# Optimization experiments

Hardware: AMD Instinct MI355X
Metric: run time of the kernel (lower is better)

Reference implementation:

```python
import jax, jax.numpy as jnp
import numpy as np

D_MODEL = 512; NHEAD = 8; D_FF = 2048
B = 8; C = 64; P = 128
HALF = D_MODEL // 2        # per-branch embed dim (256)
H_HALF = NHEAD // 2        # per-branch heads (4)
HD = HALF // H_HALF        # per-branch head dim (64)
ROPE_BASE = 10000.0
THETA_SCALE = 2.0 * np.pi
LN_EPS = 1e-5; RMS_EPS = 1e-8


def setup_inputs():
    ks = jax.random.split(jax.random.key(0), 16)
    w = lambda k, s: jax.random.normal(k, s, jnp.float32) * 0.02
    return {
        "src": jax.random.normal(ks[0], (B, C, P, D_MODEL), jnp.float32),
        "coords": jax.random.normal(ks[1], (C, 3), jnp.float32),
        "q_attn": w(ks[2], (D_MODEL,)), "rms_attn": jnp.ones((D_MODEL,), jnp.float32),
        "proj_attn_w": w(ks[3], (D_MODEL, D_MODEL)), "proj_attn_b": jnp.zeros((D_MODEL,), jnp.float32),
        "q_ffn": w(ks[4], (D_MODEL,)), "rms_ffn": jnp.ones((D_MODEL,), jnp.float32),
        "proj_ffn_w": w(ks[5], (D_MODEL, D_MODEL)), "proj_ffn_b": jnp.zeros((D_MODEL,), jnp.float32),
        "ln1_w": jnp.ones((D_MODEL,), jnp.float32), "ln1_b": jnp.zeros((D_MODEL,), jnp.float32),
        "ln2_w": jnp.ones((D_MODEL,), jnp.float32), "ln2_b": jnp.zeros((D_MODEL,), jnp.float32),
        "qkv_s_w": w(ks[6], (3 * HALF, HALF)), "qkv_s_b": jnp.zeros((3 * HALF,), jnp.float32),
        "out_s_w": w(ks[7], (HALF, HALF)), "out_s_b": jnp.zeros((HALF,), jnp.float32),
        "qkv_t_w": w(ks[8], (3 * HALF, HALF)), "qkv_t_b": jnp.zeros((3 * HALF,), jnp.float32),
        "out_t_w": w(ks[9], (HALF, HALF)), "out_t_b": jnp.zeros((HALF,), jnp.float32),
        "w1": w(ks[10], (D_FF, D_MODEL)), "b1": jnp.zeros((D_FF,), jnp.float32),
        "w2": w(ks[11], (D_MODEL, D_FF)), "b2": jnp.zeros((D_MODEL,), jnp.float32),
    }


def _rmsnorm(x, w):
    return x / jnp.sqrt(jnp.mean(x * x, axis=-1, keepdims=True) + RMS_EPS) * w


def _layernorm(x, w, b):
    m = jnp.mean(x, axis=-1, keepdims=True)
    v = jnp.mean((x - m) ** 2, axis=-1, keepdims=True)
    return (x - m) / jnp.sqrt(v + LN_EPS) * w + b


def _attn_residual(src, q, norm_w, proj_w, proj_b):
    # sources = [src] stacked on a leading n-axis (n=1) as in AttentionResidual
    V = src[None]                                  # (n, B, C, P, D)
    K = _rmsnorm(V, norm_w)
    logits = jnp.einsum('d,nbcpd->nbcp', q, K)
    wgt = jax.nn.softmax(logits, axis=0)
    out = jnp.einsum('nbcp,nbcpd->bcpd', wgt, V)
    return out @ proj_w.T + proj_b


def _build_freqs(half, dtype):
    idx = jnp.arange(half, dtype=dtype)
    return 1.0 / ROPE_BASE ** (idx / max(half, 1))


def _coord_rope(coords, half):
    # coords: (L, 3); returns cos, sin of shape (1, 1, L, half)
    axis_ids = jnp.arange(half) % 3
    c = coords - jnp.mean(coords, axis=0, keepdims=True)
    r = jnp.linalg.norm(c, axis=-1)
    c = c / jnp.maximum(jnp.max(r), 1e-6)
    freqs = _build_freqs(half, coords.dtype)
    theta = THETA_SCALE * (c[:, axis_ids] * freqs[None, :])   # (L, half)
    return jnp.cos(theta)[None, None], jnp.sin(theta)[None, None]


def _index_rope(L, half, dtype):
    freqs = _build_freqs(half, dtype)
    pos = jnp.arange(L, dtype=dtype)[:, None]
    theta = pos * freqs[None, :]                               # (L, half)
    return jnp.cos(theta)[None, None], jnp.sin(theta)[None, None]


def _apply_rope(q, k, cos, sin):
    half = q.shape[-1] // 2
    q1, q2 = q[..., :half], q[..., half:]
    k1, k2 = k[..., :half], k[..., half:]
    qr = jnp.concatenate([q1 * cos - q2 * sin, q1 * sin + q2 * cos], axis=-1)
    kr = jnp.concatenate([k1 * cos - k2 * sin, k1 * sin + k2 * cos], axis=-1)
    return qr, kr


def _mha(x, w_qkv, b_qkv, w_o, b_o, H, cos, sin):
    Bx, L, E = x.shape
    Hd = E // H
    qkv = x @ w_qkv.T + b_qkv
    q, k, v = jnp.split(qkv, 3, axis=-1)
    q = q.reshape(Bx, L, H, Hd).transpose(0, 2, 1, 3)   # (B, H, L, Hd)
    k = k.reshape(Bx, L, H, Hd).transpose(0, 2, 1, 3)
    v = v.reshape(Bx, L, H, Hd).transpose(0, 2, 1, 3)
    q, k = _apply_rope(q, k, cos, sin)
    scores = jnp.einsum('bhld,bhmd->bhlm', q, k) * (Hd ** -0.5)
    attn = jax.nn.softmax(scores, axis=-1)
    out = jnp.einsum('bhlm,bhmd->bhld', attn, v)
    out = out.transpose(0, 2, 1, 3).reshape(Bx, L, E)
    return out @ w_o.T + b_o


def reference(src, coords, q_attn, rms_attn, proj_attn_w, proj_attn_b,
              q_ffn, rms_ffn, proj_ffn_w, proj_ffn_b,
              ln1_w, ln1_b, ln2_w, ln2_b,
              qkv_s_w, qkv_s_b, out_s_w, out_s_b,
              qkv_t_w, qkv_t_b, out_t_w, out_t_b,
              w1, b1, w2, b2):
    Bx, Cx, Px, D = src.shape
    half = D // 2
    # --- attention block (pre-norm, attention-residual shortcut) ---
    res1 = _attn_residual(src, q_attn, rms_attn, proj_attn_w, proj_attn_b)
    x = _layernorm(src, ln1_w, ln1_b)
    # spatial branch: attention over channels with coordinate RoPE
    xs = x[..., :half].transpose(0, 2, 1, 3).reshape(Bx * Px, Cx, half)
    cos_s, sin_s = _coord_rope(coords, HD // 2)
    ys = _mha(xs, qkv_s_w, qkv_s_b, out_s_w, out_s_b, H_HALF, cos_s, sin_s)
    ys = ys.reshape(Bx, Px, Cx, half).transpose(0, 2, 1, 3)
    # temporal branch: attention over patches with index RoPE
    xt = x[..., half:].reshape(Bx * Cx, Px, half)
    cos_t, sin_t = _index_rope(Px, HD // 2, src.dtype)
    yt = _mha(xt, qkv_t_w, qkv_t_b, out_t_w, out_t_b, H_HALF, cos_t, sin_t)
    yt = yt.reshape(Bx, Cx, Px, half)
    x = res1 + jnp.concatenate([ys, yt], axis=-1)
    # --- FFN block ---
    res2 = _attn_residual(x, q_ffn, rms_ffn, proj_ffn_w, proj_ffn_b)
    y = _layernorm(x, ln2_w, ln2_b)
    ff = jax.nn.gelu(y @ w1.T + b1, approximate=False) @ w2.T + b2
    return res2 + ff
```

## Files before the change

### kernel.cpp

```cpp
#include <hip/hip_runtime.h>
#include <math.h>
#include <type_traits>

using u16 = unsigned short;
using u32 = unsigned int;

typedef __bf16 bf16x8 __attribute__((ext_vector_type(8)));
typedef float f32x4 __attribute__((ext_vector_type(4)));

__device__ __forceinline__ float lof(u32 u) { u32 x = u << 16; float f; __builtin_memcpy(&f, &x, 4); return f; }
__device__ __forceinline__ float hif(u32 u) { u32 x = u & 0xffff0000u; float f; __builtin_memcpy(&f, &x, 4); return f; }
__device__ __forceinline__ u16 f2bf(float f) {
  u32 u; __builtin_memcpy(&u, &f, 4);
  u32 r = u + 0x7fffu + ((u >> 16) & 1u);
  return (u16)(r >> 16);
}
__device__ __forceinline__ u32 pack2(float a, float b) { return (u32)f2bf(a) | ((u32)f2bf(b) << 16); }
__device__ __forceinline__ float bf2f(u16 s) { u32 x = ((u32)s) << 16; float f; __builtin_memcpy(&f, &x, 4); return f; }
__device__ __forceinline__ float elem(const u32* arr, int j) { u32 u = arr[j >> 1]; return (j & 1) ? hif(u) : lof(u); }

__device__ __forceinline__ void gload_lds16(const u16* g, u16* l) {
  __builtin_amdgcn_global_load_lds((const __attribute__((address_space(1))) void*)g,
                                   (__attribute__((address_space(3))) void*)l, 16, 0, 0);
}

__device__ __forceinline__ float gelu_f(float x) {
  float x3 = x * x * x;
  float u = fmaf(x3, 0.07135481283f, 1.5957691216f * x);
  float e = __expf(u);
  float r = __builtin_amdgcn_rcpf(e + 1.0f);
  return x * e * r;
}

#define NTOK 65536

#define WB_PA   0
#define WB_PF   262144
#define WB_QS   524288
#define WB_QT   720896
#define WB_OS   917504
#define WB_OT   983040
#define WB_W1   1048576
#define WB_W2F  2097152
#define WB_TOT  3407872

#define UC_US 0
#define UC_CS 768
#define UC_UT 1536
#define UC_CT 2304
#define UC_U1 3072
#define UC_C1 5120
#define UC_BC 7168

constexpr size_t O_WB  = 0;
constexpr size_t O_TAB = 6815744;
constexpr size_t O_ST1 = 6864896;
constexpr size_t O_ST2 = 7389184;
constexpr size_t O_UC  = 7913472;
constexpr size_t O_X   = 7944192;
constexpr size_t O_HB  = O_X + (size_t)NTOK * 512 * 2;

__global__ __launch_bounds__(256) void convert_weights_kernel(
    const float* __restrict__ pa, const float* __restrict__ pf,
    const float* __restrict__ qs, const float* __restrict__ qt,
    const float* __restrict__ os_, const float* __restrict__ ot,
    const float* __restrict__ w1, const float* __restrict__ w2,
    const float* __restrict__ ln1w, const float* __restrict__ ln2w,
    u16* __restrict__ dst)
{
  int i = blockIdx.x * 256 + threadIdx.x;
  if (i >= WB_TOT) return;
  float v;
  if (i < 262144)       { v = pa[i]; }
  else if (i < 524288)  { v = pf[i - 262144]; }
  else if (i < 720896)  { int l = i - 524288;  v = qs[l] * ln1w[l & 255]; }
  else if (i < 917504)  { int l = i - 720896;  v = qt[l] * ln1w[256 + (l & 255)]; }
  else if (i < 983040)  { v = os_[i - 917504]; }
  else if (i < 1048576) { v = ot[i - 983040]; }
  else if (i < 2097152) { int l = i - 1048576; v = w1[l] * ln2w[l & 511]; }
  else {
    int l = i - 2097152; int row = l / 2560, col = l - row * 2560;
    v = (col < 2048) ? w2[row * 2048 + col] : pf[row * 512 + (col - 2048)];
  }
  dst[i] = f2bf(v);
}

__global__ __launch_bounds__(256) void ucvec_kernel(
    const float* __restrict__ qs, const float* __restrict__ qt, const float* __restrict__ w1,
    const float* __restrict__ ln1w, const float* __restrict__ ln1b,
    const float* __restrict__ ln2w, const float* __restrict__ ln2b,
    const float* __restrict__ b2, const float* __restrict__ pfb,
    float* __restrict__ uc)
{
  const int j = blockIdx.x * 4 + (threadIdx.x >> 6);
  const int l = threadIdx.x & 63;
  float u = 0.f, c = 0.f;
  if (j < 768) {
#pragma unroll
    for (int q = 0; q < 4; q++) {
      int k = l * 4 + q;
      float w = qs[j * 256 + k];
      u += ln1w[k] * w; c += ln1b[k] * w;
    }
  } else if (j < 1536) {
    int jj = j - 768;
#pragma unroll
    for (int q = 0; q < 4; q++) {
      int k = l * 4 + q;
      float w = qt[jj * 256 + k];
      u += ln1w[256 + k] * w; c += ln1b[256 + k] * w;
    }
  } else if (j < 3584) {
    int jj = j - 1536;
#pragma unroll
    for (int q = 0; q < 8; q++) {
      int k = l * 8 + q;
      float w = w1[jj * 512 + k];
      u += ln2w[k] * w; c += ln2b[k] * w;
    }
  } else if (j < 4096) {
    if (l == 0) { int jj = j - 3584; uc[UC_BC + jj] = b2[jj] + pfb[jj]; }
    return;
  } else return;
#pragma unroll
  for (int o = 32; o > 0; o >>= 1) { u += __shfl_xor(u, o); c += __shfl_xor(c, o); }
  if (l == 0) {
    if (j < 768)       { uc[UC_US + j] = u;          uc[UC_CS + j] = c; }
    else if (j < 1536) { uc[UC_UT + (j - 768)] = u;  uc[UC_CT + (j - 768)] = c; }
    else               { uc[UC_U1 + (j - 1536)] = u; uc[UC_C1 + (j - 1536)] = c; }
  }
}

__global__ __launch_bounds__(256) void rope_tables_kernel(const float* __restrict__ coords, float* __restrict__ tab)
{
  __shared__ float cs[192];
  __shared__ float mean3[3];
  __shared__ float rmax;
  int t = threadIdx.x;
  if (t < 192) cs[t] = coords[t];
  __syncthreads();
  if (t < 3) { float s = 0.f; for (int i = 0; i < 64; i++) s += cs[i * 3 + t]; mean3[t] = s * (1.0f / 64.0f); }
  __syncthreads();
  if (t < 192) cs[t] -= mean3[t % 3];
  __syncthreads();
  if (t == 0) {
    float mx = 0.f;
    for (int i = 0; i < 64; i++) {
      float x = cs[i * 3], y = cs[i * 3 + 1], z = cs[i * 3 + 2];
      mx = fmaxf(mx, sqrtf(x * x + y * y + z * z));
    }
    rmax = fmaxf(mx, 1e-6f);
  }
  __syncthreads();
  float inv = 1.0f / rmax;
  for (int e = t; e < 2048; e += 256) {
    int c = e >> 5, j = e & 31;
    float freq = 1.0f / powf(10000.0f, (float)j * (1.0f / 32.0f));
    float th = 6.283185307179586f * (cs[c * 3 + (j % 3)] * inv) * freq;
    tab[e] = cosf(th); tab[2048 + e] = sinf(th);
  }
  for (int e = t; e < 4096; e += 256) {
    int p = e >> 5, j = e & 31;
    float freq = 1.0f / powf(10000.0f, (float)j * (1.0f / 32.0f));
    float th = (float)p * freq;
    tab[4096 + e] = cosf(th); tab[8192 + e] = sinf(th);
  }
}

__global__ __launch_bounds__(256) void ln_stats_f32_kernel(
    const float* __restrict__ xin, float2* __restrict__ st, u16* __restrict__ srcb)
{
  const int tok = blockIdx.x * 4 + (threadIdx.x >> 6);
  const int lane = threadIdx.x & 63;
  const float* row = xin + (size_t)tok * 512 + lane * 8;
  float4 v0 = ((const float4*)row)[0];
  float4 v1 = ((const float4*)row)[1];
  float v[8] = {v0.x, v0.y, v0.z, v0.w, v1.x, v1.y, v1.z, v1.w};
  float s = 0.f, ss = 0.f;
#pragma unroll
  for (int j = 0; j < 8; j++) { s += v[j]; ss += v[j] * v[j]; }
#pragma unroll
  for (int o = 32; o > 0; o >>= 1) { s += __shfl_xor(s, o); ss += __shfl_xor(ss, o); }
  if (lane == 0) {
    float mean = s * (1.0f / 512.0f);
    float rstd = rsqrtf(ss * (1.0f / 512.0f) - mean * mean + 1e-5f);
    st[tok] = make_float2(mean, rstd);
  }
  if (srcb) {
    uint4 o; u32* op = (u32*)&o;
#pragma unroll
    for (int d = 0; d < 4; d++) op[d] = pack2(v[2 * d], v[2 * d + 1]);
    *(uint4*)(srcb + (size_t)tok * 512 + lane * 8) = o;
  }
}

__global__ __launch_bounds__(256) void ln_stats_bf16_kernel(const u16* __restrict__ xin, float2* __restrict__ st)
{
  const int tok = blockIdx.x * 4 + (threadIdx.x >> 6);
  const int lane = threadIdx.x & 63;
  uint4 u = ((const uint4*)(xin + (size_t)tok * 512))[lane];
  u32 uu[4] = {u.x, u.y, u.z, u.w};
  float s = 0.f, ss = 0.f;
#pragma unroll
  for (int d = 0; d < 4; d++) {
    float a = lof(uu[d]), b = hif(uu[d]);
    s += a + b; ss += a * a + b * b;
  }
#pragma unroll
  for (int o = 32; o > 0; o >>= 1) { s += __shfl_xor(s, o); ss += __shfl_xor(ss, o); }
  if (lane == 0) {
    float mean = s * (1.0f / 512.0f);
    float rstd = rsqrtf(ss * (1.0f / 512.0f) - mean * mean + 1e-5f);
    st[tok] = make_float2(mean, rstd);
  }
}

template<int AMODE, int EMODE, typename OutT>
__global__ __launch_bounds__(256) void gemm128_kernel(
    const u16* __restrict__ A16, int lda,
    const u16* __restrict__ A2, int lda2,
    const u16* __restrict__ Wt, int ldw,
    OutT* __restrict__ C, int ldc,
    const float* __restrict__ bias,
    const float2* __restrict__ stats,
    const float* __restrict__ uvec, const float* __restrict__ cvec,
    int K)
{
  const int t = threadIdx.x;
  const int lane = t & 63, wid = t >> 6;
  const int wm = wid >> 1, wn = wid & 1;
  const int l15 = lane & 15, l4 = lane >> 4;

  const int ntn = gridDim.x;
  const int nwg = ntn * gridDim.y;
  int flat = blockIdx.y * ntn + blockIdx.x;
  int q = nwg >> 3, rmd = nwg & 7, xcd = flat & 7, idx = flat >> 3;
  int wg = (xcd < rmd ? xcd * (q + 1) : rmd * (q + 1) + (xcd - rmd) * q) + idx;
  const int m0 = (wg / ntn) * 128, n0 = (wg % ntn) * 128;

  f32x4 acc[4][4] = {};
  const int r0 = t >> 2;
  const size_t arow0 = (size_t)(m0 + r0);

  __shared__ u16 Asb[2][128 * 32];
  __shared__ u16 Bsb[2][128 * 32];
  const int chs = (t & 3) ^ ((t >> 3) & 3);
  const u16* Wp = Wt + (size_t)(n0 + r0) * ldw + chs * 8;
  const size_t wstep = (size_t)64 * ldw;
  const int nt = K / 32;
  auto stage = [&](int ti, int buf) {
    const int kk = ti * 32;
    const int cbk = kk + chs * 8;
    const u16* pa; size_t rstep;
    if constexpr (AMODE == 4) {
      if (kk < 2048) { pa = A16 + arow0 * lda + cbk;          rstep = (size_t)64 * lda; }
      else           { pa = A2 + arow0 * lda2 + (cbk - 2048); rstep = (size_t)64 * lda2; }
    } else {
      pa = A16 + arow0 * lda + cbk; rstep = (size_t)64 * lda;
    }
    gload_lds16(pa, &Asb[buf][t * 8]);
    gload_lds16(pa + rstep, &Asb[buf][t * 8 + 2048]);
    gload_lds16(Wp + kk, &Bsb[buf][t * 8]);
    gload_lds16(Wp + wstep + kk, &Bsb[buf][t * 8 + 2048]);
  };
  stage(0, 0);
  int cur = 0;
  const int pco = (l4 ^ ((l15 >> 1) & 3)) * 8;
  for (int ti = 0; ti < nt; ti++) {
    if (ti + 1 < nt) {
      stage(ti + 1, cur ^ 1);
      __builtin_amdgcn_sched_barrier(0);
      asm volatile("s_waitcnt vmcnt(4)" ::: "memory");
    } else {
      __builtin_amdgcn_sched_barrier(0);
      asm volatile("s_waitcnt vmcnt(0)" ::: "memory");
    }
    __builtin_amdgcn_sched_barrier(0);
    __builtin_amdgcn_s_barrier();
    __builtin_amdgcn_sched_barrier(0);
    bf16x8 af[4], bfr[4];
#pragma unroll
    for (int i = 0; i < 4; i++)
      af[i] = *(const bf16x8*)(&Asb[cur][(wm * 64 + i * 16 + l15) * 32 + pco]);
#pragma unroll
    for (int j = 0; j < 4; j++)
      bfr[j] = *(const bf16x8*)(&Bsb[cur][(wn * 64 + j * 16 + l15) * 32 + pco]);
#pragma unroll
    for (int i = 0; i < 4; i++)
#pragma unroll
      for (int j = 0; j < 4; j++)
        acc[i][j] = __builtin_amdgcn_mfma_f32_16x16x32_bf16(af[i], bfr[j], acc[i][j], 0, 0, 0);
    __builtin_amdgcn_sched_barrier(0);
    __builtin_amdgcn_s_barrier();
    __builtin_amdgcn_sched_barrier(0);
    cur ^= 1;
  }

#pragma unroll
  for (int i = 0; i < 4; i++) {
    const int row = m0 + wm * 64 + i * 16 + l4 * 4;
#pragma unroll
    for (int j = 0; j < 4; j++) {
      const int col = n0 + wn * 64 + j * 16 + l15;
      const float bv = bias[col];
#pragma unroll
      for (int rr = 0; rr < 4; rr++) {
        float v = acc[i][j][rr];
        if constexpr (EMODE >= 3) {
          float2 s = stats[row + rr];
          v = s.y * v - s.x * s.y * uvec[col] + cvec[col] + bv;
          if constexpr (EMODE == 4) v = gelu_f(v);
        } else {
          v += bv;
        }
        const size_t idxc = (size_t)(row + rr) * ldc + col;
        if constexpr (std::is_same<OutT, u16>::value) {
          if constexpr (EMODE == 2) v += bf2f(C[idxc]);
          C[idxc] = f2bf(v);
        } else {
          if constexpr (EMODE == 2) v += C[idxc];
          C[idxc] = v;
        }
      }
    }
  }
}

template<int EMODE, typename OutT>
__global__ __launch_bounds__(256) void gemm_f32a_kernel(
    const float* __restrict__ A32, int lda,
    const u16* __restrict__ Wt, int ldw,
    OutT* __restrict__ C, int ldc,
    const float* __restrict__ bias,
    const float2* __restrict__ stats,
    const float* __restrict__ uvec, const float* __restrict__ cvec,
    int K)
{
  const int t = threadIdx.x;
  const int lane = t & 63, wid = t >> 6;
  const int wm = wid >> 1, wn = wid & 1;
  const int l15 = lane & 15, l4 = lane >> 4;
  const int r0 = t >> 2;
  const int ntn = gridDim.x;
  const int nwg = ntn * gridDim.y;
  int flat = blockIdx.y * ntn + blockIdx.x;
  int q = nwg >> 3, rmd = nwg & 7, xcd = flat & 7, idx = flat >> 3;
  int wg = (xcd < rmd ? xcd * (q + 1) : rmd * (q + 1) + (xcd - rmd) * q) + idx;
  const int m0 = (wg / ntn) * 128, n0 = (wg % ntn) * 128;
  f32x4 acc[4][4] = {};
  const size_t arow0 = (size_t)(m0 + r0);
  const int ch = t & 3;
  const u16* Wp = Wt + (size_t)(n0 + r0) * ldw + ch * 8;
  const size_t wstep = (size_t)64 * ldw;
  __shared__ u16 As[128 * 40];
  __shared__ u16 Bs[128 * 32];
  for (int k0 = 0; k0 < K; k0 += 32) {
    const int cbx = k0 + ch * 8;
    uint4 a0, a1;
    float f0[8], f1[8];
    float4 x0 = *(const float4*)(A32 + arow0 * lda + cbx);
    float4 x1 = *(const float4*)(A32 + arow0 * lda + cbx + 4);
    float4 y0 = *(const float4*)(A32 + (arow0 + 64) * lda + cbx);
    float4 y1 = *(const float4*)(A32 + (arow0 + 64) * lda + cbx + 4);
    f0[0]=x0.x; f0[1]=x0.y; f0[2]=x0.z; f0[3]=x0.w; f0[4]=x1.x; f0[5]=x1.y; f0[6]=x1.z; f0[7]=x1.w;
    f1[0]=y0.x; f1[1]=y0.y; f1[2]=y0.z; f1[3]=y0.w; f1[4]=y1.x; f1[5]=y1.y; f1[6]=y1.z; f1[7]=y1.w;
    u32* p0 = (u32*)&a0; u32* p1 = (u32*)&a1;
#pragma unroll
    for (int d = 0; d < 4; d++) { p0[d] = pack2(f0[2*d], f0[2*d+1]); p1[d] = pack2(f1[2*d], f1[2*d+1]); }
    __syncthreads();
    gload_lds16(Wp + k0, Bs + t * 8);
    gload_lds16(Wp + wstep + k0, Bs + t * 8 + 2048);
    *(uint4*)(As + r0 * 40 + ch * 8) = a0;
    *(uint4*)(As + (r0 + 64) * 40 + ch * 8) = a1;
    __syncthreads();
    bf16x8 af[4], bfr[4];
#pragma unroll
    for (int i = 0; i < 4; i++)
      af[i] = *(const bf16x8*)(As + (wm * 64 + i * 16 + l15) * 40 + l4 * 8);
#pragma unroll
    for (int j = 0; j < 4; j++)
      bfr[j] = *(const bf16x8*)(Bs + (wn * 64 + j * 16 + l15) * 32 + l4 * 8);
#pragma unroll
    for (int i = 0; i < 4; i++)
#pragma unroll
      for (int j = 0; j < 4; j++)
        acc[i][j] = __builtin_amdgcn_mfma_f32_16x16x32_bf16(af[i], bfr[j], acc[i][j], 0, 0, 0);
  }
#pragma unroll
  for (int i = 0; i < 4; i++) {
    const int row = m0 + wm * 64 + i * 16 + l4 * 4;
#pragma unroll
    for (int j = 0; j < 4; j++) {
      const int col = n0 + wn * 64 + j * 16 + l15;
      const float bv = bias[col];
#pragma unroll
      for (int rr = 0; rr < 4; rr++) {
        float v = acc[i][j][rr];
        if constexpr (EMODE == 3) {
          float2 s = stats[row + rr];
          v = s.y * v - s.x * s.y * uvec[col] + cvec[col] + bv;
        } else {
          v += bv;
        }
        const size_t idxc = (size_t)(row + rr) * ldc + col;
        if constexpr (std::is_same<OutT, u16>::value) C[idxc] = f2bf(v);
        else C[idxc] = v;
      }
    }
  }
}

template<int L>
__global__ __launch_bounds__(256) void attn_mfma_kernel(
    const u16* __restrict__ qkv,
    u16* __restrict__ aout,
    const float* __restrict__ tab)
{
  constexpr int KP = 72;
  constexpr int PP = L + 8;
  constexpr int VP = L + 8;
  constexpr int NI = L / 64;
  constexpr int NJ = L / 16;
  constexpr int NK = L / 32;
  __shared__ u16 Ks[L * KP];
  __shared__ u16 Vt[64 * VP];
  __shared__ u16 Ps[L * PP];

  const int t = threadIdx.x;
  const int lane = t & 63;
  const int w = t >> 6;
  const int l15 = lane & 15, l4 = lane >> 4;
  const int sq = blockIdx.x, h = blockIdx.y;

  long base; int tstride; const float *ct, *st;
  if constexpr (L == 64) { base = (long)(sq >> 7) * 8192 + (sq & 127); tstride = 128; ct = tab;        st = tab + 2048; }
  else                   { base = (long)sq * 128;                      tstride = 1;   ct = tab + 4096; st = tab + 8192; }

  {
    const int tok = t >> 1, hh = t & 1;
    if (tok < L) {
      const size_t rb = (size_t)(base + (long)tok * tstride) * 768 + h * 64;
      u32 ku[32];
#pragma unroll
      for (int i = 0; i < 8; i++) ((uint4*)ku)[i] = ((const uint4*)(qkv + rb + 256))[i];
      const float* cc = ct + tok * 32;
      const float* ss = st + tok * 32;
      u32* kd = (u32*)(Ks + tok * KP + hh * 32);
#pragma unroll
      for (int jj = 0; jj < 16; jj++) {
        float c0 = cc[2*jj], s0 = ss[2*jj], c1 = cc[2*jj+1], s1 = ss[2*jj+1];
        float a0 = elem(ku, 2*jj),     b0 = elem(ku, 2*jj+32);
        float a1 = elem(ku, 2*jj+1),   b1 = elem(ku, 2*jj+33);
        float r0v = hh ? (a0*s0 + b0*c0) : (a0*c0 - b0*s0);
        float r1v = hh ? (a1*s1 + b1*c1) : (a1*c1 - b1*s1);
        kd[jj] = pack2(r0v, r1v);
      }
      u32 vu[16];
#pragma unroll
      for (int i = 0; i < 4; i++) ((uint4*)vu)[i] = ((const uint4*)(qkv + rb + 512 + hh * 32))[i];
#pragma unroll
      for (int j = 0; j < 32; j++)
        Vt[(hh * 32 + j) * VP + tok] = (u16)(vu[j >> 1] >> ((j & 1) * 16));
    }
  }

  bf16x8 aq[NI][2];
#pragma unroll
  for (int i = 0; i < NI; i++) {
    const int row = w * (16 * NI) + i * 16 + l15;
    const u16* qr = qkv + (size_t)(base + (long)row * tstride) * 768 + h * 64;
    uint4 ua = *(const uint4*)(qr + l4 * 8);
    uint4 ub = *(const uint4*)(qr + 32 + l4 * 8);
    u32 au[4] = {ua.x, ua.y, ua.z, ua.w};
    u32 bu[4] = {ub.x, ub.y, ub.z, ub.w};
    const float* cc = ct + row * 32 + l4 * 8;
    const float* ss = st + row * 32 + l4 * 8;
    u32 q0[4], q1[4];
#pragma unroll
    for (int d = 0; d < 4; d++) {
      float a0 = lof(au[d]), a1 = hif(au[d]);
      float b0 = lof(bu[d]), b1 = hif(bu[d]);
      float c0 = cc[2*d], c1 = cc[2*d+1], s0 = ss[2*d], s1 = ss[2*d+1];
      q0[d] = pack2(a0*c0 - b0*s0, a1*c1 - b1*s1);
      q1[d] = pack2(a0*s0 + b0*c0, a1*s1 + b1*c1);
    }
    __builtin_memcpy(&aq[i][0], q0, 16);
    __builtin_memcpy(&aq[i][1], q1, 16);
  }
  __syncthreads();

  f32x4 acc[NI][NJ] = {};
#pragma unroll
  for (int j = 0; j < NJ; j++) {
#pragma unroll
    for (int kk = 0; kk < 2; kk++) {
      bf16x8 bk = *(const bf16x8*)(Ks + (j * 16 + l15) * KP + kk * 32 + l4 * 8);
#pragma unroll
      for (int i = 0; i < NI; i++)
        acc[i][j] = __builtin_amdgcn_mfma_f32_16x16x32_bf16(aq[i][kk], bk, acc[i][j], 0, 0, 0);
    }
  }

  float inv_[NI][4];
#pragma unroll
  for (int i = 0; i < NI; i++) {
#pragma unroll
    for (int rr = 0; rr < 4; rr++) {
      float m = acc[i][0][rr];
#pragma unroll
      for (int j = 1; j < NJ; j++) m = fmaxf(m, acc[i][j][rr]);
      m = fmaxf(m, __shfl_xor(m, 1)); m = fmaxf(m, __shfl_xor(m, 2));
      m = fmaxf(m, __shfl_xor(m, 4)); m = fmaxf(m, __shfl_xor(m, 8));
      m *= 0.125f;
      const int qrow = w * (16 * NI) + i * 16 + l4 * 4 + rr;
      float sm = 0.f;
#pragma unroll
      for (int j = 0; j < NJ; j++) {
        float e = __expf(acc[i][j][rr] * 0.125f - m);
        sm += e;
        Ps[qrow * PP + j * 16 + l15] = f2bf(e);
      }
      sm += __shfl_xor(sm, 1); sm += __shfl_xor(sm, 2);
      sm += __shfl_xor(sm, 4); sm += __shfl_xor(sm, 8);
      inv_[i][rr] = 1.0f / sm;
    }
  }

  f32x4 o[NI][4] = {};
#pragma unroll
  for (int kk = 0; kk < NK; kk++) {
    bf16x8 pa[NI];
#pragma unroll
    for (int i = 0; i < NI; i++)
      pa[i] = *(const bf16x8*)(Ps + (w * (16 * NI) + i * 16 + l15) * PP + kk * 32 + l4 * 8);
#pragma unroll
    for (int jn = 0; jn < 4; jn++) {
      bf16x8 bv = *(const bf16x8*)(Vt + (jn * 16 + l15) * VP + kk * 32 + l4 * 8);
#pragma unroll
      for (int i = 0; i < NI; i++)
        o[i][jn] = __builtin_amdgcn_mfma_f32_16x16x32_bf16(pa[i], bv, o[i][jn], 0, 0, 0);
    }
  }

#pragma unroll
  for (int i = 0; i < NI; i++) {
#pragma unroll
    for (int rr = 0; rr < 4; rr++) {
      const int qrow = w * (16 * NI) + i * 16 + l4 * 4 + rr;
      u16* op = aout + (size_t)(base + (long)qrow * tstride) * 256 + h * 64;
      const float iv = inv_[i][rr];
#pragma unroll
      for (int jn = 0; jn < 4; jn++)
        op[jn * 16 + l15] = f2bf(o[i][jn][rr] * iv);
    }
  }
}

extern "C" void kernel_launch(void* const* d_in, const int* in_sizes, int n_in,
                              void* d_out, int out_size, void* d_ws, size_t ws_size,
                              hipStream_t stream) {
  const float* src         = (const float*)d_in[0];
  const float* coords      = (const float*)d_in[1];
  const float* proj_attn_w = (const float*)d_in[4];
  const float* proj_attn_b = (const float*)d_in[5];
  const float* proj_ffn_w  = (const float*)d_in[8];
  const float* proj_ffn_b  = (const float*)d_in[9];
  const float* ln1_w = (const float*)d_in[10];
  const float* ln1_b = (const float*)d_in[11];
  const float* ln2_w = (const float*)d_in[12];
  const float* ln2_b = (const float*)d_in[13];
  const float* qkv_s_w = (const float*)d_in[14];
  const float* qkv_s_b = (const float*)d_in[15];
  const float* out_s_w = (const float*)d_in[16];
  const float* out_s_b = (const float*)d_in[17];
  const float* qkv_t_w = (const float*)d_in[18];
  const float* qkv_t_b = (const float*)d_in[19];
  const float* out_t_w = (const float*)d_in[20];
  const float* out_t_b = (const float*)d_in[21];
  const float* w1 = (const float*)d_in[22];
  const float* b1 = (const float*)d_in[23];
  const float* w2 = (const float*)d_in[24];
  const float* b2 = (const float*)d_in[25];
  float* out = (float*)d_out;
  char* ws = (char*)d_ws;

  const size_t srcb_bytes = (size_t)NTOK * 512 * 2;
  const int tiers[6] = {32768, 16384, 8192, 4096, 2048, 512};
  int crows = 0; bool fast = false;
  for (int i = 0; i < 6; i++) {
    size_t need = O_HB + (size_t)tiers[i] * 2048 * 2 + srcb_bytes;
    if (ws_size >= need) { crows = tiers[i]; fast = true; break; }
  }
  if (!crows) {
    for (int i = 0; i < 6; i++)
      if (ws_size >= O_HB + (size_t)tiers[i] * 2048 * 2) { crows = tiers[i]; break; }
  }
  if (!crows) return;
  size_t o_srcb = O_HB + (size_t)crows * 2048 * 2;

  u16*    wb  = (u16*)(ws + O_WB);
  float*  tab = (float*)(ws + O_TAB);
  float2* st1 = (float2*)(ws + O_ST1);
  float2* st2 = (float2*)(ws + O_ST2);
  float*  uc  = (float*)(ws + O_UC);
  u16*    x   = (u16*)(ws + O_X);
  u16*    hb  = (u16*)(ws + O_HB);
  u16*    srcb = fast ? (u16*)(ws + o_srcb) : nullptr;

  u16* qkvb  = (u16*)d_out;
  u16* aoutb = (u16*)((char*)d_out + (size_t)NTOK * 768 * 2);

  convert_weights_kernel<<<(WB_TOT + 255) / 256, 256, 0, stream>>>(
      proj_attn_w, proj_ffn_w, qkv_s_w, qkv_t_w, out_s_w, out_t_w, w1, w2, ln1_w, ln2_w, wb);
  ucvec_kernel<<<1024, 256, 0, stream>>>(qkv_s_w, qkv_t_w, w1, ln1_w, ln1_b, ln2_w, ln2_b, b2, proj_ffn_b, uc);
  rope_tables_kernel<<<1, 256, 0, stream>>>(coords, tab);
  ln_stats_f32_kernel<<<NTOK / 4, 256, 0, stream>>>(src, st1, srcb);

  if (fast)
    gemm128_kernel<0, 0, u16><<<dim3(4, 512), 256, 0, stream>>>(srcb, 512, nullptr, 0, wb + WB_PA, 512, x, 512, proj_attn_b, nullptr, nullptr, nullptr, 512);
  else
    gemm_f32a_kernel<0, u16><<<dim3(4, 512), 256, 0, stream>>>(src, 512, wb + WB_PA, 512, x, 512, proj_attn_b, nullptr, nullptr, nullptr, 512);

  if (fast)
    gemm128_kernel<0, 3, u16><<<dim3(6, 512), 256, 0, stream>>>(srcb, 512, nullptr, 0, wb + WB_QS, 256, qkvb, 768, qkv_s_b, st1, uc + UC_US, uc + UC_CS, 256);
  else
    gemm_f32a_kernel<3, u16><<<dim3(6, 512), 256, 0, stream>>>(src, 512, wb + WB_QS, 256, qkvb, 768, qkv_s_b, st1, uc + UC_US, uc + UC_CS, 256);
  attn_mfma_kernel<64><<<dim3(1024, 4), 256, 0, stream>>>(qkvb, aoutb, tab);
  gemm128_kernel<0, 2, u16><<<dim3(2, 512), 256, 0, stream>>>(aoutb, 256, nullptr, 0, wb + WB_OS, 256, x, 512, out_s_b, nullptr, nullptr, nullptr, 256);

  if (fast)
    gemm128_kernel<0, 3, u16><<<dim3(6, 512), 256, 0, stream>>>(srcb + 256, 512, nullptr, 0, wb + WB_QT, 256, qkvb, 768, qkv_t_b, st1, uc + UC_UT, uc + UC_CT, 256);
  else
    gemm_f32a_kernel<3, u16><<<dim3(6, 512), 256, 0, stream>>>(src + 256, 512, wb + WB_QT, 256, qkvb, 768, qkv_t_b, st1, uc + UC_UT, uc + UC_CT, 256);
  attn_mfma_kernel<128><<<dim3(512, 4), 256, 0, stream>>>(qkvb, aoutb, tab);
  gemm128_kernel<0, 2, u16><<<dim3(2, 512), 256, 0, stream>>>(aoutb, 256, nullptr, 0, wb + WB_OT, 256, x + 256, 512, out_t_b, nullptr, nullptr, nullptr, 256);

  ln_stats_bf16_kernel<<<NTOK / 4, 256, 0, stream>>>(x, st2);

  for (int r = 0; r < NTOK; r += crows) {
    gemm128_kernel<0, 4, u16><<<dim3(16, crows / 128), 256, 0, stream>>>(
        x + (size_t)r * 512, 512, nullptr, 0, wb + WB_W1, 512, hb, 2048, b1, st2 + r, uc + UC_U1, uc + UC_C1, 512);
    gemm128_kernel<4, 0, float><<<dim3(4, crows / 128), 256, 0, stream>>>(
        hb, 2048, x + (size_t)r * 512, 512, wb + WB_W2F, 2560, out + (size_t)r * 512, 512, uc + UC_BC, nullptr, nullptr, nullptr, 2560);
  }
}
```

Before: 1.013 ms.

## Use 256x256 tiled GEMM with register-direct B loads for FFN layers

Adds a 512-thread GEMM kernel that computes 256x256 output tiles (8x4 MFMA accumulators per wave). A is staged into LDS, while B fragments are loaded straight from global memory into registers and double-buffered. Both FFN GEMMs now use this kernel, and a larger row-chunk tier (65536) is added so the FFN can run in fewer chunks when the workspace is big enough. The larger tile is meant to raise arithmetic intensity and cut LDS traffic for B. In exchange, the kernel uses far more registers and launches fewer workgroups, and B reads from global memory are not staged through LDS.

```diff
diff --git a/kernel.cpp b/kernel.cpp
--- a/kernel.cpp
+++ b/kernel.cpp
@@ -250,14 +250,8 @@
   const int nt = K / 32;
   auto stage = [&](int ti, int buf) {
     const int kk = ti * 32;
-    const int cbk = kk + chs * 8;
-    const u16* pa; size_t rstep;
-    if constexpr (AMODE == 4) {
-      if (kk < 2048) { pa = A16 + arow0 * lda + cbk;          rstep = (size_t)64 * lda; }
-      else           { pa = A2 + arow0 * lda2 + (cbk - 2048); rstep = (size_t)64 * lda2; }
-    } else {
-      pa = A16 + arow0 * lda + cbk; rstep = (size_t)64 * lda;
-    }
+    const u16* pa = A16 + arow0 * lda + kk + chs * 8;
+    const size_t rstep = (size_t)64 * lda;
     gload_lds16(pa, &Asb[buf][t * 8]);
     gload_lds16(pa + rstep, &Asb[buf][t * 8 + 2048]);
     gload_lds16(Wp + kk, &Bsb[buf][t * 8]);
@@ -309,7 +303,6 @@
         if constexpr (EMODE >= 3) {
           float2 s = stats[row + rr];
           v = s.y * v - s.x * s.y * uvec[col] + cvec[col] + bv;
-          if constexpr (EMODE == 4) v = gelu_f(v);
         } else {
           v += bv;
         }
@@ -321,6 +314,128 @@
           if constexpr (EMODE == 2) v += C[idxc];
           C[idxc] = v;
         }
+      }
+    }
+  }
+}
+
+template<int AMODE, int EMODE, typename OutT>
+__global__ __launch_bounds__(512, 1) void gemm2r_kernel(
+    const u16* __restrict__ A16, int lda,
+    const u16* __restrict__ A2, int lda2,
+    const u16* __restrict__ Wt, int ldw,
+    OutT* __restrict__ C, int ldc,
+    const float* __restrict__ bias,
+    const float2* __restrict__ stats,
+    const float* __restrict__ uvec, const float* __restrict__ cvec,
+    int K)
+{
+  __shared__ u16 As[2][256 * 32];
+  const int t = threadIdx.x;
+  const int lane = t & 63, wid = t >> 6;
+  const int wm = wid >> 2, wn = wid & 3;
+  const int l15 = lane & 15, l4 = lane >> 4;
+  const int chs = (t & 3) ^ ((t >> 3) & 3);
+
+  const int ntn = gridDim.x;
+  const int nwg = ntn * gridDim.y;
+  int flat = blockIdx.y * ntn + blockIdx.x;
+  int q = nwg >> 3, rmd = nwg & 7, xcd = flat & 7, idx = flat >> 3;
+  int wg = (xcd < rmd ? xcd * (q + 1) : rmd * (q + 1) + (xcd - rmd) * q) + idx;
+  const int m0 = (wg / ntn) * 256, n0 = (wg % ntn) * 256;
+
+  f32x4 acc[8][4] = {};
+
+  const int srow = t >> 2;
+  const size_t arow0 = (size_t)(m0 + srow);
+  const u16* Bbase = Wt + (size_t)(n0 + wn * 64 + l15) * ldw + l4 * 8;
+  const size_t bjstep = (size_t)16 * ldw;
+
+  auto stageA = [&](int ti, int buf) {
+    const int kk = ti << 5;
+    const int cbk = kk + chs * 8;
+    const u16* pa; size_t rstep;
+    if constexpr (AMODE == 4) {
+      if (kk < 2048) { pa = A16 + arow0 * lda + cbk;          rstep = (size_t)128 * lda; }
+      else           { pa = A2 + arow0 * lda2 + (cbk - 2048); rstep = (size_t)128 * lda2; }
+    } else {
+      pa = A16 + arow0 * lda + cbk; rstep = (size_t)128 * lda;
+    }
+    gload_lds16(pa,         &As[buf][t * 8]);
+    gload_lds16(pa + rstep, &As[buf][t * 8 + 4096]);
+  };
+  auto loadB = [&](int ti, bf16x8* b) {
+    const u16* p = Bbase + (ti << 5);
+#pragma unroll
+    for (int j = 0; j < 4; j++)
+      b[j] = *(const bf16x8*)(p + (size_t)j * bjstep);
+  };
+
+  const int pco = (l4 ^ ((l15 >> 1) & 3)) * 8;
+  const int nt = K >> 5;
+  bf16x8 bA[4], bB[4];
+  stageA(0, 0);
+  loadB(0, bA);
+
+  for (int ti = 0; ti < nt; ti += 2) {
+    __builtin_amdgcn_sched_barrier(0);
+    asm volatile("s_waitcnt vmcnt(4)" ::: "memory");
+    __builtin_amdgcn_sched_barrier(0);
+    __builtin_amdgcn_s_barrier();
+    __builtin_amdgcn_sched_barrier(0);
+    if (ti + 1 < nt) { stageA(ti + 1, 1); loadB(ti + 1, bB); }
+    {
+      bf16x8 af[8];
+#pragma unroll
+      for (int i = 0; i < 8; i++)
+        af[i] = *(const bf16x8*)(&As[0][(wm * 128 + i * 16 + l15) * 32 + pco]);
+#pragma unroll
+      for (int i = 0; i < 8; i++)
+#pragma unroll
+        for (int j = 0; j < 4; j++)
+          acc[i][j] = __builtin_amdgcn_mfma_f32_16x16x32_bf16(af[i], bA[j], acc[i][j], 0, 0, 0);
+    }
+    __builtin_amdgcn_sched_barrier(0);
+    if (ti + 2 < nt) { asm volatile("s_waitcnt vmcnt(4)" ::: "memory"); }
+    else             { asm volatile("s_waitcnt vmcnt(0)" ::: "memory"); }
+    __builtin_amdgcn_sched_barrier(0);
+    __builtin_amdgcn_s_barrier();
+    __builtin_amdgcn_sched_barrier(0);
+    if (ti + 2 < nt) { stageA(ti + 2, 0); loadB(ti + 2, bA); }
+    {
+      bf16x8 af[8];
+#pragma unroll
+      for (int i = 0; i < 8; i++)
+        af[i] = *(const bf16x8*)(&As[1][(wm * 128 + i * 16 + l15) * 32 + pco]);
+#pragma unroll
+      for (int i = 0; i < 8; i++)
+#pragma unroll
+        for (int j = 0; j < 4; j++)
+          acc[i][j] = __builtin_amdgcn_mfma_f32_16x16x32_bf16(af[i], bB[j], acc[i][j], 0, 0, 0);
+    }
+    __builtin_amdgcn_sched_barrier(0);
+  }
+
+#pragma unroll
+  for (int i = 0; i < 8; i++) {
+    const int row = m0 + wm * 128 + i * 16 + l4 * 4;
+#pragma unroll
+    for (int j = 0; j < 4; j++) {
+      const int col = n0 + wn * 64 + j * 16 + l15;
+      const float bv = bias[col];
+#pragma unroll
+      for (int rr = 0; rr < 4; rr++) {
+        float v = acc[i][j][rr];
+        if constexpr (EMODE == 4) {
+          float2 s = stats[row + rr];
+          v = s.y * v - s.x * s.y * uvec[col] + cvec[col] + bv;
+          v = gelu_f(v);
+        } else {
+          v += bv;
+        }
+        const size_t idxc = (size_t)(row + rr) * ldc + col;
+        if constexpr (std::is_same<OutT, u16>::value) C[idxc] = f2bf(v);
+        else C[idxc] = v;
       }
     }
   }
@@ -585,14 +700,14 @@
   char* ws = (char*)d_ws;
 
   const size_t srcb_bytes = (size_t)NTOK * 512 * 2;
-  const int tiers[6] = {32768, 16384, 8192, 4096, 2048, 512};
+  const int tiers[7] = {65536, 32768, 16384, 8192, 4096, 2048, 512};
   int crows = 0; bool fast = false;
-  for (int i = 0; i < 6; i++) {
+  for (int i = 0; i < 7; i++) {
     size_t need = O_HB + (size_t)tiers[i] * 2048 * 2 + srcb_bytes;
     if (ws_size >= need) { crows = tiers[i]; fast = true; break; }
   }
   if (!crows) {
-    for (int i = 0; i < 6; i++)
+    for (int i = 0; i < 7; i++)
       if (ws_size >= O_HB + (size_t)tiers[i] * 2048 * 2) { crows = tiers[i]; break; }
   }
   if (!crows) return;
@@ -638,9 +753,9 @@
   ln_stats_bf16_kernel<<<NTOK / 4, 256, 0, stream>>>(x, st2);
 
   for (int r = 0; r < NTOK; r += crows) {
-    gemm128_kernel<0, 4, u16><<<dim3(16, crows / 128), 256, 0, stream>>>(
+    gemm2r_kernel<0, 4, u16><<<dim3(8, crows / 256), 512, 0, stream>>>(
         x + (size_t)r * 512, 512, nullptr, 0, wb + WB_W1, 512, hb, 2048, b1, st2 + r, uc + UC_U1, uc + UC_C1, 512);
-    gemm128_kernel<4, 0, float><<<dim3(4, crows / 128), 256, 0, stream>>>(
+    gemm2r_kernel<4, 0, float><<<dim3(2, crows / 256), 512, 0, stream>>>(
         hb, 2048, x + (size_t)r * 512, 512, wb + WB_W2F, 2560, out + (size_t)r * 512, 512, uc + UC_BC, nullptr, nullptr, nullptr, 2560);
   }
 }
```

After: 1.016 ms. Within noise of the previous version (+0.3%).
